# Kernel optimization log

Hardware: AMD Instinct MI355X
Metric: run time of the kernel (lower is better)

The kernel has to match this reference:

```python
import jax, jax.numpy as jnp
import numpy as np

B, T, D = 2, 2048, 2048
H, HD = 8, 128
C = H * HD  # 1024 channels
BT = 64     # chunk size
EPS_RMS = 1.1920929e-07  # torch fp32 finfo eps (RMSNorm default)


def causal_dw_conv(x, w, b):
    # x: [B,T,C], w: [C,4], b: [C]. Equals torch Conv1d(groups=C, k=4, padding=3)[..., :T]
    Bx, Tx, Cx = x.shape
    xp = jnp.pad(x, ((0, 0), (3, 0), (0, 0)))
    out = sum(xp[:, j:j + Tx, :] * w[None, None, :, j] for j in range(4))
    return out + b


def chunk_kda(q, k, v, g):
    # q,k,g: [B,H,T,K]; v: [B,H,T,V]
    Bx, Hx, Tx, K = q.shape
    V = v.shape[-1]
    NT = Tx // BT
    resh = lambda a: a.reshape(Bx, Hx, NT, BT, a.shape[-1])
    q, k, v, g = map(resh, (q, k, v, g))
    gc = jnp.cumsum(g, axis=-2)                        # [B,H,NT,BT,K]
    diff = gc[..., :, None, :] - gc[..., None, :, :]   # [B,H,NT,BT,BT,K]
    tri_incl = jnp.tril(jnp.ones((BT, BT), bool))
    tri_strict = jnp.tril(jnp.ones((BT, BT), bool), -1)
    Aqk = jnp.einsum('bhnik,bhnjk,bhnijk->bhnij', q, k, jnp.exp(diff)) * tri_incl
    Akk = jnp.einsum('bhnik,bhnjk,bhnijk->bhnij', k, k, jnp.exp(-diff)) * tri_strict
    # UT transform: the in-place forward substitution in the source computes
    # A = (I + strictly_lower(Akk))^{-1}; apply it via a unit-lower triangular solve.
    M = Akk + jnp.eye(BT, dtype=q.dtype)
    rhs = jnp.concatenate([jnp.exp(gc) * k, v], axis=-1)
    sol = jax.scipy.linalg.solve_triangular(M, rhs, lower=True, unit_diagonal=True)
    w_, u = sol[..., :K], sol[..., K:]                 # w = A@(exp(gc)*k), u = A@v
    qg = q * jnp.exp(gc)

    def step(S, xs):
        qg_i, k_i, u_i, gc_i, w_i, Aqk_i = xs
        o_i = qg_i @ S + Aqk_i @ (u_i - w_i @ S)
        g_last = gc_i[:, :, -1]                        # [B,H,K]
        decay = jnp.exp(g_last[:, :, None, :] - gc_i)  # [B,H,BT,K]
        S = S * jnp.exp(g_last)[..., :, None] + jnp.einsum('bhck,bhcv->bhkv', k_i * decay, u_i)
        return S, o_i

    xs = tuple(jnp.moveaxis(a, 2, 0) for a in (qg, k, u, gc, w_, Aqk))
    S0 = jnp.zeros((Bx, Hx, K, V), q.dtype)
    S, o = jax.lax.scan(step, S0, xs)
    o = jnp.moveaxis(o, 0, 2).reshape(Bx, Hx, Tx, V)
    return o, S


def _forward(x, Wq, Wk, Wv, conv_q_w, conv_q_b, conv_k_w, conv_k_b, conv_v_w, conv_v_b,
             Wad, Wau, Wb, Wgd, Wgu, norm_w, Wo):
    Bx, Tx, Dx = x.shape
    heads = lambda y: y.reshape(Bx, Tx, H, HD).transpose(0, 2, 1, 3)
    q = heads(causal_dw_conv(x @ Wq, conv_q_w, conv_q_b))
    k = heads(causal_dw_conv(x @ Wk, conv_k_w, conv_k_b))
    q = q / jnp.maximum(jnp.linalg.norm(q, axis=-1, keepdims=True), 1e-12)
    k = k / jnp.maximum(jnp.linalg.norm(k, axis=-1, keepdims=True), 1e-12)
    v = heads(jax.nn.silu(causal_dw_conv(x @ Wv, conv_v_w, conv_v_b)))
    alpha = jax.nn.sigmoid(heads(x @ Wad @ Wau))
    g = jnp.log(jnp.clip(alpha, 1e-6, None))
    _beta = jax.nn.sigmoid(x @ Wb)  # computed in source but unused by chunk_kda
    o, S = chunk_kda(q, k, v, g)
    o = o.transpose(0, 2, 1, 3)                        # [B,T,H,HD]
    o = o * jax.lax.rsqrt(jnp.mean(o * o, axis=-1, keepdims=True) + EPS_RMS) * norm_w
    gate = jax.nn.sigmoid(x @ Wgd @ Wgu).reshape(Bx, Tx, H, HD)
    o = (o * gate).reshape(Bx, Tx, H * HD)
    return o @ Wo, S


def setup_inputs():
    key = jax.random.key(0)
    ks = jax.random.split(key, 16)
    n = lambda k, shape, s=0.02: jax.random.normal(k, shape, jnp.float32) * s
    return {
        'x': jax.random.normal(ks[0], (B, T, D), jnp.float32),
        'Wq': n(ks[1], (D, C)), 'Wk': n(ks[2], (D, C)), 'Wv': n(ks[3], (D, C)),
        'conv_q_w': n(ks[4], (C, 4), 0.1), 'conv_q_b': jnp.zeros((C,), jnp.float32),
        'conv_k_w': n(ks[5], (C, 4), 0.1), 'conv_k_b': jnp.zeros((C,), jnp.float32),
        'conv_v_w': n(ks[6], (C, 4), 0.1), 'conv_v_b': jnp.zeros((C,), jnp.float32),
        'Wad': n(ks[7], (D, HD)), 'Wau': n(ks[8], (HD, C)),
        'Wb': n(ks[9], (D, H)),
        'Wgd': n(ks[10], (D, HD)), 'Wgu': n(ks[11], (HD, C)),
        'norm_w': jnp.ones((HD,), jnp.float32),
        'Wo': n(ks[12], (C, D)),
    }


def reference(x, Wq, Wk, Wv, conv_q_w, conv_q_b, conv_k_w, conv_k_b, conv_v_w, conv_v_b,
              Wad, Wau, Wb, Wgd, Wgu, norm_w, Wo):
    return _forward(x, Wq, Wk, Wv, conv_q_w, conv_q_b, conv_k_w, conv_k_b, conv_v_w, conv_v_b,
                    Wad, Wau, Wb, Wgd, Wgu, norm_w, Wo)
```

## Files before the change

kernel.cpp:

```cpp
#include <hip/hip_runtime.h>
#include <hip/hip_bf16.h>
#include <cstdint>
#include <cstddef>

constexpr int B_  = 2;
constexpr int T_  = 2048;
constexpr int D_  = 2048;
constexpr int H_  = 8;
constexpr int HD_ = 128;
constexpr int C_  = 1024;
constexpr int BT_ = 64;
constexpr int NT_ = 32;
constexpr int M_  = 4096;
constexpr float EPS_RMS = 1.1920929e-07f;

typedef __bf16 bf16x8 __attribute__((ext_vector_type(8)));
typedef float f32x4 __attribute__((ext_vector_type(4)));

typedef const __attribute__((address_space(1))) unsigned int* gptr_t;
typedef __attribute__((address_space(3))) unsigned int* lptr_t;

__device__ __forceinline__ void gload16(const void* g, void* l) {
  __builtin_amdgcn_global_load_lds((gptr_t)g, (lptr_t)l, 16, 0, 0);
}

template <typename OutT>
__global__ __launch_bounds__(256) void gemm_bf16k(
    const __hip_bfloat16* __restrict__ A, const __hip_bfloat16* __restrict__ Bt,
    OutT* __restrict__ C, int N, int K) {
  __shared__ __hip_bfloat16 sA[128 * 32];
  __shared__ __hip_bfloat16 sB[128 * 32];
  const int tid = threadIdx.x;
  const int lane = tid & 63;
  const int m0 = blockIdx.y * 128, n0 = blockIdx.x * 128;
  const int wm = ((tid >> 6) >> 1) * 64, wn = ((tid >> 6) & 1) * 64;
  f32x4 acc[4][4];
#pragma unroll
  for (int i = 0; i < 4; ++i)
#pragma unroll
    for (int j = 0; j < 4; ++j) acc[i][j] = (f32x4)(0.f);
  const int f0 = tid, f1 = tid + 256;
  const int r0 = f0 >> 2, c0 = (f0 & 3) * 8;
  const int r1 = f1 >> 2, c1 = (f1 & 3) * 8;
  const size_t aoff0 = (size_t)(m0 + r0) * K + c0;
  const size_t aoff1 = (size_t)(m0 + r1) * K + c1;
  const size_t boff0 = (size_t)(n0 + r0) * K + c0;
  const size_t boff1 = (size_t)(n0 + r1) * K + c1;
  const int lr = lane & 15, lk = (lane >> 4) * 8;
  for (int k0 = 0; k0 < K; k0 += 32) {
    __syncthreads();
    gload16(A + aoff0 + k0, &sA[f0 * 8]);
    gload16(A + aoff1 + k0, &sA[f1 * 8]);
    gload16(Bt + boff0 + k0, &sB[f0 * 8]);
    gload16(Bt + boff1 + k0, &sB[f1 * 8]);
    __syncthreads();
    bf16x8 af[4], bfr[4];
#pragma unroll
    for (int i = 0; i < 4; ++i)
      af[i] = *(const bf16x8*)&sA[(wm + i * 16 + lr) * 32 + lk];
#pragma unroll
    for (int j = 0; j < 4; ++j)
      bfr[j] = *(const bf16x8*)&sB[(wn + j * 16 + lr) * 32 + lk];
#pragma unroll
    for (int i = 0; i < 4; ++i)
#pragma unroll
      for (int j = 0; j < 4; ++j)
        acc[i][j] = __builtin_amdgcn_mfma_f32_16x16x32_bf16(af[i], bfr[j], acc[i][j], 0, 0, 0);
  }
  const int er = (lane >> 4) * 4, ec = lane & 15;
#pragma unroll
  for (int i = 0; i < 4; ++i) {
#pragma unroll
    for (int j = 0; j < 4; ++j) {
      int row = m0 + wm + i * 16 + er;
      int col = n0 + wn + j * 16 + ec;
#pragma unroll
      for (int r = 0; r < 4; ++r) {
        float v = acc[i][j][r];
        if constexpr (sizeof(OutT) == 2)
          C[(size_t)(row + r) * N + col] = __float2bfloat16(v);
        else
          C[(size_t)(row + r) * N + col] = v;
      }
    }
  }
}

__global__ __launch_bounds__(256) void gemm_p1(
    const __hip_bfloat16* __restrict__ xb, const __hip_bfloat16* __restrict__ Wt_qkv,
    const __hip_bfloat16* __restrict__ Wt_dg, __hip_bfloat16* __restrict__ pre_qkv,
    float* __restrict__ slabs) {
  __shared__ __hip_bfloat16 sA[128 * 32];
  __shared__ __hip_bfloat16 sB[128 * 32];
  const int bid = blockIdx.x;
  const int tid = threadIdx.x;
  const int lane = tid & 63;
  const bool isqkv = bid < 768;
  int m0, n0, kb, ke, N, z = 0;
  const __hip_bfloat16* Bt;
  if (isqkv) {
    n0 = (bid % 24) * 128; m0 = (bid / 24) * 128;
    kb = 0; ke = 2048; N = 3072; Bt = Wt_qkv;
  } else {
    int s = bid - 768;
    n0 = (s & 1) * 128; m0 = ((s >> 1) & 31) * 128;
    z = s >> 6;
    kb = z * 512; ke = kb + 512; N = 256; Bt = Wt_dg;
  }
  const int K = 2048;
  const int wm = ((tid >> 6) >> 1) * 64, wn = ((tid >> 6) & 1) * 64;
  f32x4 acc[4][4];
#pragma unroll
  for (int i = 0; i < 4; ++i)
#pragma unroll
    for (int j = 0; j < 4; ++j) acc[i][j] = (f32x4)(0.f);
  const int f0 = tid, f1 = tid + 256;
  const int r0 = f0 >> 2, c0 = (f0 & 3) * 8;
  const int r1 = f1 >> 2, c1 = (f1 & 3) * 8;
  const size_t aoff0 = (size_t)(m0 + r0) * K + c0;
  const size_t aoff1 = (size_t)(m0 + r1) * K + c1;
  const size_t boff0 = (size_t)(n0 + r0) * K + c0;
  const size_t boff1 = (size_t)(n0 + r1) * K + c1;
  const int lr = lane & 15, lk = (lane >> 4) * 8;
  for (int k0 = kb; k0 < ke; k0 += 32) {
    __syncthreads();
    gload16(xb + aoff0 + k0, &sA[f0 * 8]);
    gload16(xb + aoff1 + k0, &sA[f1 * 8]);
    gload16(Bt + boff0 + k0, &sB[f0 * 8]);
    gload16(Bt + boff1 + k0, &sB[f1 * 8]);
    __syncthreads();
    bf16x8 af[4], bfr[4];
#pragma unroll
    for (int i = 0; i < 4; ++i)
      af[i] = *(const bf16x8*)&sA[(wm + i * 16 + lr) * 32 + lk];
#pragma unroll
    for (int j = 0; j < 4; ++j)
      bfr[j] = *(const bf16x8*)&sB[(wn + j * 16 + lr) * 32 + lk];
#pragma unroll
    for (int i = 0; i < 4; ++i)
#pragma unroll
      for (int j = 0; j < 4; ++j)
        acc[i][j] = __builtin_amdgcn_mfma_f32_16x16x32_bf16(af[i], bfr[j], acc[i][j], 0, 0, 0);
  }
  const int er = (lane >> 4) * 4, ec = lane & 15;
  if (isqkv) {
#pragma unroll
    for (int i = 0; i < 4; ++i)
#pragma unroll
      for (int j = 0; j < 4; ++j) {
        int row = m0 + wm + i * 16 + er;
        int col = n0 + wn + j * 16 + ec;
#pragma unroll
        for (int r = 0; r < 4; ++r)
          pre_qkv[(size_t)(row + r) * N + col] = __float2bfloat16(acc[i][j][r]);
      }
  } else {
    float* Cs = slabs + (size_t)z * M_ * 256;
#pragma unroll
    for (int i = 0; i < 4; ++i)
#pragma unroll
      for (int j = 0; j < 4; ++j) {
        int row = m0 + wm + i * 16 + er;
        int col = n0 + wn + j * 16 + ec;
#pragma unroll
        for (int r = 0; r < 4; ++r)
          Cs[(size_t)(row + r) * N + col] = acc[i][j][r];
      }
  }
}

__global__ __launch_bounds__(256) void gemm_augu(
    const __hip_bfloat16* __restrict__ ad, const __hip_bfloat16* __restrict__ gd,
    const __hip_bfloat16* __restrict__ Wau, const __hip_bfloat16* __restrict__ Wgu,
    float* __restrict__ a_full, __hip_bfloat16* __restrict__ gatef) {
  constexpr int N = 1024, K = 128;
  const int z = blockIdx.z;
  const __hip_bfloat16* A = z ? gd : ad;
  const __hip_bfloat16* Bt = z ? Wgu : Wau;
  __shared__ __hip_bfloat16 sA[128 * 32];
  __shared__ __hip_bfloat16 sB[128 * 32];
  const int tid = threadIdx.x;
  const int lane = tid & 63;
  const int m0 = blockIdx.y * 128, n0 = blockIdx.x * 128;
  const int wm = ((tid >> 6) >> 1) * 64, wn = ((tid >> 6) & 1) * 64;
  f32x4 acc[4][4];
#pragma unroll
  for (int i = 0; i < 4; ++i)
#pragma unroll
    for (int j = 0; j < 4; ++j) acc[i][j] = (f32x4)(0.f);
  const int f0 = tid, f1 = tid + 256;
  const int r0 = f0 >> 2, c0 = (f0 & 3) * 8;
  const int r1 = f1 >> 2, c1 = (f1 & 3) * 8;
  const size_t aoff0 = (size_t)(m0 + r0) * K + c0;
  const size_t aoff1 = (size_t)(m0 + r1) * K + c1;
  const size_t boff0 = (size_t)(n0 + r0) * K + c0;
  const size_t boff1 = (size_t)(n0 + r1) * K + c1;
  const int lr = lane & 15, lk = (lane >> 4) * 8;
#pragma unroll
  for (int k0 = 0; k0 < K; k0 += 32) {
    __syncthreads();
    gload16(A + aoff0 + k0, &sA[f0 * 8]);
    gload16(A + aoff1 + k0, &sA[f1 * 8]);
    gload16(Bt + boff0 + k0, &sB[f0 * 8]);
    gload16(Bt + boff1 + k0, &sB[f1 * 8]);
    __syncthreads();
    bf16x8 af[4], bfr[4];
#pragma unroll
    for (int i = 0; i < 4; ++i)
      af[i] = *(const bf16x8*)&sA[(wm + i * 16 + lr) * 32 + lk];
#pragma unroll
    for (int j = 0; j < 4; ++j)
      bfr[j] = *(const bf16x8*)&sB[(wn + j * 16 + lr) * 32 + lk];
#pragma unroll
    for (int i = 0; i < 4; ++i)
#pragma unroll
      for (int j = 0; j < 4; ++j)
        acc[i][j] = __builtin_amdgcn_mfma_f32_16x16x32_bf16(af[i], bfr[j], acc[i][j], 0, 0, 0);
  }
  const int er = (lane >> 4) * 4, ec = lane & 15;
#pragma unroll
  for (int i = 0; i < 4; ++i)
#pragma unroll
    for (int j = 0; j < 4; ++j) {
      int row = m0 + wm + i * 16 + er;
      int col = n0 + wn + j * 16 + ec;
#pragma unroll
      for (int r = 0; r < 4; ++r) {
        float v = acc[i][j][r];
        if (z == 0) a_full[(size_t)(row + r) * N + col] = v;
        else        gatef[(size_t)(row + r) * N + col] = __float2bfloat16(v);
      }
    }
}

__global__ __launch_bounds__(256) void reduce_dg(
    const float* __restrict__ slabs, __hip_bfloat16* __restrict__ adb,
    __hip_bfloat16* __restrict__ gdb) {
  int idx = blockIdx.x * 256 + threadIdx.x;
  int m = idx >> 8, c = idx & 255;
  const size_t ss = (size_t)M_ * 256;
  float s = slabs[idx] + slabs[idx + ss] + slabs[idx + 2 * ss] + slabs[idx + 3 * ss];
  if (c < 128) adb[(size_t)m * 128 + c] = __float2bfloat16(s);
  else         gdb[(size_t)m * 128 + (c - 128)] = __float2bfloat16(s);
}

__global__ __launch_bounds__(256) void prep(
    const float* __restrict__ x, const float* __restrict__ Wq,
    const float* __restrict__ Wk, const float* __restrict__ Wv,
    const float* __restrict__ Wad, const float* __restrict__ Wgd,
    const float* __restrict__ Wau, const float* __restrict__ Wgu,
    const float* __restrict__ Wo, __hip_bfloat16* __restrict__ xb,
    __hip_bfloat16* __restrict__ Wt_qkv, __hip_bfloat16* __restrict__ Wt_dg,
    __hip_bfloat16* __restrict__ Wt_aug, __hip_bfloat16* __restrict__ Wt_o) {
  __shared__ float tile[32][33];
  int bid = blockIdx.x;
  const int tid = threadIdx.x;
  if (bid < 8192) {
    size_t i = ((size_t)bid * 256 + tid) * 4;
    float4 v = *(const float4*)(x + i);
    xb[i + 0] = __float2bfloat16(v.x);
    xb[i + 1] = __float2bfloat16(v.y);
    xb[i + 2] = __float2bfloat16(v.z);
    xb[i + 3] = __float2bfloat16(v.w);
    return;
  }
  bid -= 8192;
  const float* W; __hip_bfloat16* dst; int K, N, bx, by;
  if (bid < 6144) {
    int z = bid / 2048, r = bid % 2048;
    W = (z == 0) ? Wq : (z == 1) ? Wk : Wv;
    dst = Wt_qkv + (size_t)z * C_ * D_;
    K = D_; N = C_; bx = r & 31; by = r >> 5;
  } else if (bid < 6144 + 512) {
    int b2 = bid - 6144;
    int z = b2 >> 8, r = b2 & 255;
    W = z ? Wgd : Wad;
    dst = Wt_dg + (size_t)z * HD_ * D_;
    K = D_; N = HD_; bx = r & 3; by = r >> 2;
  } else if (bid < 6144 + 512 + 256) {
    int b2 = bid - 6144 - 512;
    int z = b2 >> 7, r = b2 & 127;
    W = z ? Wgu : Wau;
    dst = Wt_aug + (size_t)z * C_ * HD_;
    K = HD_; N = C_; bx = r & 31; by = r >> 5;
  } else {
    int b2 = bid - 6144 - 512 - 256;
    W = Wo; dst = Wt_o;
    K = C_; N = D_; bx = b2 & 63; by = b2 >> 6;
  }
  int tx = tid & 31, ty = tid >> 5;
  int kb = by * 32, nb = bx * 32;
#pragma unroll
  for (int s = 0; s < 4; ++s) {
    int kk = ty + s * 8;
    tile[kk][tx] = W[(size_t)(kb + kk) * N + nb + tx];
  }
  __syncthreads();
#pragma unroll
  for (int s = 0; s < 4; ++s) {
    int nn = ty + s * 8;
    dst[(size_t)(nb + nn) * K + kb + tx] = __float2bfloat16(tile[tx][nn]);
  }
}

__global__ __launch_bounds__(256) void gc_lds(
    const float* __restrict__ a_full, float* __restrict__ gc,
    float* __restrict__ glast) {
  __shared__ float gcS[64][128];
  const int tid = threadIdx.x;
  const int bhn = blockIdx.x;
  const int bh = bhn >> 5, n = bhn & 31;
  const int b = bh >> 3, h = bh & 7;
  const int t0 = n * 64, hoff = h * 128;
  for (int ci = tid; ci < 2048; ci += 256) {
    int r = ci >> 5, c4 = (ci & 31) * 4;
    *(float4*)&gcS[r][c4] =
        *(const float4*)(a_full + (size_t)(b * T_ + t0 + r) * C_ + hoff + c4);
  }
  __syncthreads();
  if (tid < 128) {
    float run = 0.f;
    for (int i = 0; i < 64; ++i) {
      float a = gcS[i][tid];
      float s = fmaxf(1.f / (1.f + __expf(-a)), 1e-6f);
      run += __logf(s);
      gcS[i][tid] = run;
    }
    glast[(size_t)bhn * 128 + tid] = run;
  }
  __syncthreads();
  const size_t gbase = ((size_t)bh * T_ + t0) * 128;
  for (int ci = tid; ci < 2048; ci += 256) {
    int r = ci >> 5, c4 = (ci & 31) * 4;
    *(float4*)(gc + gbase + r * 128 + c4) = *(const float4*)&gcS[r][c4];
  }
}

__global__ __launch_bounds__(128) void conv_qkv(
    const __hip_bfloat16* __restrict__ pre, const float* __restrict__ gc,
    const float* __restrict__ cqw, const float* __restrict__ cqb,
    const float* __restrict__ ckw, const float* __restrict__ ckb,
    const float* __restrict__ cvw, const float* __restrict__ cvb,
    __hip_bfloat16* __restrict__ qg, __hip_bfloat16* __restrict__ kp,
    __hip_bfloat16* __restrict__ km, __hip_bfloat16* __restrict__ vb) {
  int idx = blockIdx.x;
  int h = idx & 7;
  int t = (idx >> 3) & (T_ - 1);
  int b = idx >> 14;
  int d = threadIdx.x;
  int c = h * HD_ + d;
  const __hip_bfloat16* p = pre + (size_t)(b * T_ + t) * (3 * C_) + c;
  float aq, ak, av;
  {
    float w0 = cqw[c * 4], w1 = cqw[c * 4 + 1], w2 = cqw[c * 4 + 2], w3 = cqw[c * 4 + 3];
    aq = cqb[c] + w3 * __bfloat162float(p[0]);
    if (t > 0) aq += w2 * __bfloat162float(p[-(ptrdiff_t)(3 * C_)]);
    if (t > 1) aq += w1 * __bfloat162float(p[-2 * (ptrdiff_t)(3 * C_)]);
    if (t > 2) aq += w0 * __bfloat162float(p[-3 * (ptrdiff_t)(3 * C_)]);
  }
  {
    const __hip_bfloat16* pk = p + C_;
    float w0 = ckw[c * 4], w1 = ckw[c * 4 + 1], w2 = ckw[c * 4 + 2], w3 = ckw[c * 4 + 3];
    ak = ckb[c] + w3 * __bfloat162float(pk[0]);
    if (t > 0) ak += w2 * __bfloat162float(pk[-(ptrdiff_t)(3 * C_)]);
    if (t > 1) ak += w1 * __bfloat162float(pk[-2 * (ptrdiff_t)(3 * C_)]);
    if (t > 2) ak += w0 * __bfloat162float(pk[-3 * (ptrdiff_t)(3 * C_)]);
  }
  {
    const __hip_bfloat16* pv = p + 2 * C_;
    float w0 = cvw[c * 4], w1 = cvw[c * 4 + 1], w2 = cvw[c * 4 + 2], w3 = cvw[c * 4 + 3];
    av = cvb[c] + w3 * __bfloat162float(pv[0]);
    if (t > 0) av += w2 * __bfloat162float(pv[-(ptrdiff_t)(3 * C_)]);
    if (t > 1) av += w1 * __bfloat162float(pv[-2 * (ptrdiff_t)(3 * C_)]);
    if (t > 2) av += w0 * __bfloat162float(pv[-3 * (ptrdiff_t)(3 * C_)]);
  }
  float ssq = aq * aq, ssk = ak * ak;
#pragma unroll
  for (int o = 1; o < 64; o <<= 1) {
    ssq += __shfl_xor(ssq, o);
    ssk += __shfl_xor(ssk, o);
  }
  __shared__ float red[2][2];
  if ((d & 63) == 0) { red[0][d >> 6] = ssq; red[1][d >> 6] = ssk; }
  __syncthreads();
  float nq = fmaxf(sqrtf(red[0][0] + red[0][1]), 1e-12f);
  float nk = fmaxf(sqrtf(red[1][0] + red[1][1]), 1e-12f);
  size_t oi = (((size_t)b * H_ + h) * T_ + t) * HD_ + d;
  float g = gc[oi];
  float eg = __expf(g), emg = __expf(-g);
  qg[oi] = __float2bfloat16(aq / nq * eg);
  float kn = ak / nk;
  kp[oi] = __float2bfloat16(kn * eg);
  km[oi] = __float2bfloat16(kn * emg);
  vb[oi] = __float2bfloat16(av * (1.f / (1.f + __expf(-av))));
}

__global__ __launch_bounds__(256) void chunk_mid(
    const __hip_bfloat16* __restrict__ qg, const __hip_bfloat16* __restrict__ kp,
    const __hip_bfloat16* __restrict__ km, const __hip_bfloat16* __restrict__ vb,
    __hip_bfloat16* __restrict__ Aq, __hip_bfloat16* __restrict__ w_bf,
    __hip_bfloat16* __restrict__ u_bf, __hip_bfloat16* __restrict__ PT_bf) {
  __shared__ float A_T[64][68];
  __shared__ float solu[64][128];
  const int tid = threadIdx.x;
  const int bhn = blockIdx.x;
  const size_t gbase = ((size_t)(bhn >> 5) * T_ + (size_t)(bhn & 31) * BT_) * HD_;
  const int wv = tid >> 6, lane = tid & 63;
  const int lr = lane & 15, lg = lane >> 4;
  const int prod = wv >> 1, rh = wv & 1;

  {
    const __hip_bfloat16* A = (prod ? qg : km) + gbase;
    const __hip_bfloat16* Bt = (prod ? km : kp) + gbase;
    f32x4 acc[2][4];
#pragma unroll
    for (int i = 0; i < 2; ++i)
#pragma unroll
      for (int j = 0; j < 4; ++j) acc[i][j] = (f32x4)(0.f);
#pragma unroll
    for (int k0 = 0; k0 < 128; k0 += 32) {
      bf16x8 af[2], bfr[4];
#pragma unroll
      for (int i = 0; i < 2; ++i)
        af[i] = *(const bf16x8*)(A + (size_t)(rh * 32 + i * 16 + lr) * 128 + k0 + lg * 8);
#pragma unroll
      for (int j = 0; j < 4; ++j)
        bfr[j] = *(const bf16x8*)(Bt + (size_t)(j * 16 + lr) * 128 + k0 + lg * 8);
#pragma unroll
      for (int i = 0; i < 2; ++i)
#pragma unroll
        for (int j = 0; j < 4; ++j)
          acc[i][j] = __builtin_amdgcn_mfma_f32_16x16x32_bf16(af[i], bfr[j], acc[i][j], 0, 0, 0);
    }
    if (prod == 0) {
#pragma unroll
      for (int i = 0; i < 2; ++i)
#pragma unroll
        for (int j = 0; j < 4; ++j) {
          int row0 = rh * 32 + i * 16 + lg * 4;
          int col = j * 16 + lr;
          *(float4*)&A_T[col][row0] =
              make_float4(acc[i][j][0], acc[i][j][1], acc[i][j][2], acc[i][j][3]);
        }
    } else {
      __hip_bfloat16* dst = Aq + (size_t)bhn * 4096;
#pragma unroll
      for (int i = 0; i < 2; ++i)
#pragma unroll
        for (int j = 0; j < 4; ++j)
#pragma unroll
          for (int r = 0; r < 4; ++r) {
            int row = rh * 32 + i * 16 + lg * 4 + r;
            int col = j * 16 + lr;
            float v = (col <= row) ? acc[i][j][r] : 0.f;
            dst[row * 64 + col] = __float2bfloat16(v);
          }
    }
  }
  __syncthreads();

  {
    const int col = tid & 127;
    const __hip_bfloat16* rhs = ((tid < 128) ? kp : vb) + gbase;
    float s[64];
#pragma unroll
    for (int i = 0; i < 64; ++i)
      s[i] = __bfloat162float(rhs[(size_t)i * 128 + col]);
#pragma unroll
    for (int i = 0; i < 63; ++i) {
      const float si = s[i];
      const int j0 = (i + 1) & ~3;
#pragma unroll
      for (int j4 = j0; j4 < 64; j4 += 4) {
        float4 a4 = *(const float4*)&A_T[i][j4];
        if (j4 > i)     s[j4]     -= a4.x * si;
        if (j4 + 1 > i) s[j4 + 1] -= a4.y * si;
        if (j4 + 2 > i) s[j4 + 2] -= a4.z * si;
        if (j4 + 3 > i) s[j4 + 3] -= a4.w * si;
      }
    }
    if (tid < 128) {
#pragma unroll
      for (int i = 0; i < 64; ++i)
        w_bf[gbase + (size_t)i * 128 + col] = __float2bfloat16(s[i]);
    } else {
#pragma unroll
      for (int i = 0; i < 64; ++i) {
        u_bf[gbase + (size_t)i * 128 + col] = __float2bfloat16(s[i]);
        solu[i][col] = s[i];
      }
    }
  }
  __syncthreads();

  {
    const int kd0 = (tid >> 4) * 8, vd0 = (tid & 15) * 8;
    float acc[8][8];
#pragma unroll
    for (int a = 0; a < 8; ++a)
#pragma unroll
      for (int b2 = 0; b2 < 8; ++b2) acc[a][b2] = 0.f;
    for (int i = 0; i < 64; ++i) {
      uint4 rawv = *(const uint4*)(km + gbase + (size_t)i * 128 + kd0);
      const __hip_bfloat16* hp = (const __hip_bfloat16*)&rawv;
      float kv[8];
#pragma unroll
      for (int e = 0; e < 8; ++e) kv[e] = __bfloat162float(hp[e]);
      float uv[8];
      *(float4*)(uv)     = *(const float4*)&solu[i][vd0];
      *(float4*)(uv + 4) = *(const float4*)&solu[i][vd0 + 4];
#pragma unroll
      for (int a = 0; a < 8; ++a)
#pragma unroll
        for (int b2 = 0; b2 < 8; ++b2) acc[a][b2] = fmaf(kv[a], uv[b2], acc[a][b2]);
    }
    __hip_bfloat16* dst = PT_bf + (size_t)bhn * 16384;
#pragma unroll
    for (int b2 = 0; b2 < 8; ++b2) {
      union { __hip_bfloat16 hx[8]; uint4 u4; } pk2;
#pragma unroll
      for (int a = 0; a < 8; ++a) pk2.hx[a] = __float2bfloat16(acc[a][b2]);
      *(uint4*)(dst + (size_t)(vd0 + b2) * 128 + kd0) = pk2.u4;
    }
  }
}

__global__ __launch_bounds__(128) void scan_pt(
    const __hip_bfloat16* __restrict__ PT_bf, const float* __restrict__ glast,
    __hip_bfloat16* __restrict__ STg, float* __restrict__ Sout) {
  int vd = blockIdx.x & 127;
  int bh = blockIdx.x >> 7;
  int kd = threadIdx.x;
  float s = 0.f;
  for (int n = 0; n < NT_; ++n) {
    size_t idx = (((size_t)bh * NT_ + n) * HD_ + vd) * HD_ + kd;
    float p = __bfloat162float(PT_bf[idx]);
    STg[idx] = __float2bfloat16(s);
    float gl = glast[((size_t)bh * NT_ + n) * 128 + kd];
    s = (s + p) * __expf(gl);
  }
  Sout[((size_t)bh * HD_ + kd) * HD_ + vd] = s;
}

__global__ __launch_bounds__(256) void chunk_tail(
    const __hip_bfloat16* __restrict__ qg_bf, const __hip_bfloat16* __restrict__ w_bf,
    const __hip_bfloat16* __restrict__ u_bf, const __hip_bfloat16* __restrict__ Aq_bf,
    const __hip_bfloat16* __restrict__ STg, const __hip_bfloat16* __restrict__ gatef,
    const float* __restrict__ normw, __hip_bfloat16* __restrict__ o2b) {
  constexpr int XTS = 72;
  __shared__ __hip_bfloat16 XT[128 * XTS];
  __shared__ float red[64][4];
  const int tid = threadIdx.x;
  const int bhn = blockIdx.x;
  const int bh = bhn >> 5, n = bhn & 31;
  const int b = bh >> 3, h = bh & 7;
  const int t0 = n * 64, hoff = h * 128;
  const size_t gbase = ((size_t)bh * T_ + t0) * 128;
  const __hip_bfloat16* Sg = STg + (size_t)bhn * 16384;

  const int wv = tid >> 6, lane = tid & 63;
  const int lr = lane & 15, lg = lane >> 4;
  f32x4 accX[4][2], accO[4][2];
#pragma unroll
  for (int i = 0; i < 4; ++i)
#pragma unroll
    for (int j = 0; j < 2; ++j) { accX[i][j] = (f32x4)(0.f); accO[i][j] = (f32x4)(0.f); }

  const __hip_bfloat16* wrow = w_bf + gbase;
  const __hip_bfloat16* qrow = qg_bf + gbase;
#pragma unroll
  for (int k0 = 0; k0 < 128; k0 += 32) {
    bf16x8 aW[4], aQ[4], bS[2];
#pragma unroll
    for (int i = 0; i < 4; ++i) {
      aW[i] = *(const bf16x8*)(wrow + (size_t)(i * 16 + lr) * 128 + k0 + lg * 8);
      aQ[i] = *(const bf16x8*)(qrow + (size_t)(i * 16 + lr) * 128 + k0 + lg * 8);
    }
#pragma unroll
    for (int j = 0; j < 2; ++j)
      bS[j] = *(const bf16x8*)(Sg + (size_t)(wv * 32 + j * 16 + lr) * 128 + k0 + lg * 8);
#pragma unroll
    for (int i = 0; i < 4; ++i)
#pragma unroll
      for (int j = 0; j < 2; ++j) {
        accX[i][j] = __builtin_amdgcn_mfma_f32_16x16x32_bf16(aW[i], bS[j], accX[i][j], 0, 0, 0);
        accO[i][j] = __builtin_amdgcn_mfma_f32_16x16x32_bf16(aQ[i], bS[j], accO[i][j], 0, 0, 0);
      }
  }

#pragma unroll
  for (int i = 0; i < 4; ++i)
#pragma unroll
    for (int j = 0; j < 2; ++j) {
      int row0 = i * 16 + lg * 4;
      int col = wv * 32 + j * 16 + lr;
      union { __hip_bfloat16 hx[4]; uint2 u2; } xv;
#pragma unroll
      for (int r = 0; r < 4; ++r) {
        float uu = __bfloat162float(u_bf[gbase + (size_t)(row0 + r) * 128 + col]);
        xv.hx[r] = __float2bfloat16(uu - accX[i][j][r]);
      }
      *(uint2*)&XT[col * XTS + row0] = xv.u2;
    }
  __syncthreads();

  const __hip_bfloat16* aqb = Aq_bf + (size_t)bhn * 4096;
#pragma unroll
  for (int k0 = 0; k0 < 64; k0 += 32) {
    bf16x8 aA[4], bX[2];
#pragma unroll
    for (int i = 0; i < 4; ++i)
      aA[i] = *(const bf16x8*)(aqb + (size_t)(i * 16 + lr) * 64 + k0 + lg * 8);
#pragma unroll
    for (int j = 0; j < 2; ++j)
      bX[j] = *(const bf16x8*)&XT[(wv * 32 + j * 16 + lr) * XTS + k0 + lg * 8];
#pragma unroll
    for (int i = 0; i < 4; ++i)
#pragma unroll
      for (int j = 0; j < 2; ++j)
        accO[i][j] = __builtin_amdgcn_mfma_f32_16x16x32_bf16(aA[i], bX[j], accO[i][j], 0, 0, 0);
  }

#pragma unroll
  for (int i = 0; i < 4; ++i)
#pragma unroll
    for (int r = 0; r < 4; ++r) {
      int row = i * 16 + lg * 4 + r;
      float o0 = accO[i][0][r], o1 = accO[i][1][r];
      float ss = o0 * o0 + o1 * o1;
#pragma unroll
      for (int o = 1; o < 16; o <<= 1) ss += __shfl_xor(ss, o);
      if (lr == 0) red[row][wv] = ss;
    }
  __syncthreads();
  float nw0 = normw[wv * 32 + lr];
  float nw1 = normw[wv * 32 + 16 + lr];
#pragma unroll
  for (int i = 0; i < 4; ++i)
#pragma unroll
    for (int r = 0; r < 4; ++r) {
      int row = i * 16 + lg * 4 + r;
      float tot = red[row][0] + red[row][1] + red[row][2] + red[row][3];
      float rms = rsqrtf(tot * (1.f / 128.f) + EPS_RMS);
      size_t orow = (size_t)(b * T_ + t0 + row) * C_ + hoff;
      int c0 = wv * 32 + lr, c1 = c0 + 16;
      float g0 = __bfloat162float(gatef[orow + c0]);
      float g1 = __bfloat162float(gatef[orow + c1]);
      float s0 = 1.f / (1.f + __expf(-g0));
      float s1 = 1.f / (1.f + __expf(-g1));
      o2b[orow + c0] = __float2bfloat16(accO[i][0][r] * rms * nw0 * s0);
      o2b[orow + c1] = __float2bfloat16(accO[i][1][r] * rms * nw1 * s1);
    }
}

extern "C" void kernel_launch(void* const* d_in, const int* in_sizes, int n_in,
                              void* d_out, int out_size, void* d_ws, size_t ws_size,
                              hipStream_t stream) {
  (void)in_sizes; (void)n_in; (void)out_size;
  const float* x    = (const float*)d_in[0];
  const float* Wq   = (const float*)d_in[1];
  const float* Wk   = (const float*)d_in[2];
  const float* Wv   = (const float*)d_in[3];
  const float* cqw  = (const float*)d_in[4];
  const float* cqb  = (const float*)d_in[5];
  const float* ckw  = (const float*)d_in[6];
  const float* ckb  = (const float*)d_in[7];
  const float* cvw  = (const float*)d_in[8];
  const float* cvb  = (const float*)d_in[9];
  const float* Wad  = (const float*)d_in[10];
  const float* Wau  = (const float*)d_in[11];
  const float* Wgd  = (const float*)d_in[13];
  const float* Wgu  = (const float*)d_in[14];
  const float* normw= (const float*)d_in[15];
  const float* Wo   = (const float*)d_in[16];

  float* outp = (float*)d_out;
  float* Sout = outp + (size_t)M_ * D_;

  const size_t SZ = (size_t)M_ * C_;

  float* ws = (float*)d_ws;
  __hip_bfloat16* pre_qkv = (__hip_bfloat16*)(ws);
  float* a_full = ws + 3 * SZ / 2;
  __hip_bfloat16* gatef = (__hip_bfloat16*)(ws + 5 * SZ / 2);
  float* gc_g = ws + 3 * SZ;
  __hip_bfloat16* qg_bf = (__hip_bfloat16*)(ws + 4 * SZ);
  __hip_bfloat16* kp_bf = (__hip_bfloat16*)(ws + 9 * SZ / 2);
  __hip_bfloat16* km_bf = (__hip_bfloat16*)(ws + 5 * SZ);
  __hip_bfloat16* v_bf  = (__hip_bfloat16*)(ws + 11 * SZ / 2);
  __hip_bfloat16* w_bf  = (__hip_bfloat16*)(ws + 6 * SZ);
  __hip_bfloat16* u_bf  = (__hip_bfloat16*)(ws + 13 * SZ / 2);
  __hip_bfloat16* Aq_bf = (__hip_bfloat16*)(ws + 7 * SZ);
  float* glast = ws + 29 * SZ / 4;
  __hip_bfloat16* PT_bf = (__hip_bfloat16*)(ws + 15 * SZ / 2);
  __hip_bfloat16* STg   = (__hip_bfloat16*)(ws + 17 * SZ / 2);
  __hip_bfloat16* xb    = (__hip_bfloat16*)(ws + 19 * SZ / 2);
  __hip_bfloat16* Wt_qkv = (__hip_bfloat16*)(ws + 21 * SZ / 2);
  size_t off = 21 * SZ / 2 + 3 * SZ / 4;
  __hip_bfloat16* Wt_dg  = (__hip_bfloat16*)(ws + off); off += 262144;
  __hip_bfloat16* Wt_aug = (__hip_bfloat16*)(ws + off); off += 131072;
  __hip_bfloat16* Wt_o   = (__hip_bfloat16*)(ws + off); off += 1048576;
  __hip_bfloat16* ad_bf  = (__hip_bfloat16*)(ws + off); off += 262144;
  __hip_bfloat16* gd_bf  = (__hip_bfloat16*)(ws + off); off += 262144;
  if (ws_size < off * sizeof(float)) return;

  float* slabs = ws + 15 * SZ / 2;
  __hip_bfloat16* o2b = (__hip_bfloat16*)a_full;
  __hip_bfloat16* Wt_au = Wt_aug;
  __hip_bfloat16* Wt_gu = Wt_aug + (size_t)C_ * HD_;

  prep<<<17152, 256, 0, stream>>>(x, Wq, Wk, Wv, Wad, Wgd, Wau, Wgu, Wo,
                                  xb, Wt_qkv, Wt_dg, Wt_aug, Wt_o);

  gemm_p1<<<1024, 256, 0, stream>>>(xb, Wt_qkv, Wt_dg, pre_qkv, slabs);
  reduce_dg<<<(int)((size_t)M_ * 256 / 256), 256, 0, stream>>>(slabs, ad_bf, gd_bf);
  gemm_augu<<<dim3(C_ / 128, M_ / 128, 2), 256, 0, stream>>>(
      ad_bf, gd_bf, Wt_au, Wt_gu, a_full, gatef);

  gc_lds<<<B_ * H_ * NT_, 256, 0, stream>>>(a_full, gc_g, glast);
  conv_qkv<<<B_ * T_ * H_, 128, 0, stream>>>(pre_qkv, gc_g, cqw, cqb, ckw, ckb,
                                             cvw, cvb, qg_bf, kp_bf, km_bf, v_bf);

  chunk_mid<<<B_ * H_ * NT_, 256, 0, stream>>>(qg_bf, kp_bf, km_bf, v_bf,
                                               Aq_bf, w_bf, u_bf, PT_bf);
  scan_pt<<<B_ * H_ * HD_, 128, 0, stream>>>(PT_bf, glast, STg, Sout);

  chunk_tail<<<B_ * H_ * NT_, 256, 0, stream>>>(qg_bf, w_bf, u_bf, Aq_bf, STg,
                                                gatef, normw, o2b);
  gemm_bf16k<float><<<dim3(D_ / 128, M_ / 128), 256, 0, stream>>>(o2b, Wt_o, outp, D_, C_);
}
```

Before: 401.8 us.

## Replace projection GEMM and split-K reduce with fused 256x256 pipelined kernel

The QKV projection and the low-rank down-projections (ad/gd) now run as one 4096x3328x2048 GEMM. It uses 256x256 tiles, 8 waves, 128KB of double-buffered swizzled LDS, direct global-to-LDS loads interleaved with MFMA phases, and s_setprio scheduling. This removes the split-K fp32 slab writes, the separate reduce kernel, and the small-tile 128x128 single-buffered loop. The B pointer reads 3328 rows from Wt_qkv, so it depends on Wt_dg being laid out contiguously after Wt_qkv in the workspace (which the offsets appear to satisfy). It also launches only 208 blocks at one block per CU.

```diff
diff --git a/kernel.cpp b/kernel.cpp
--- a/kernel.cpp
+++ b/kernel.cpp
@@ -22,6 +22,176 @@
 
 __device__ __forceinline__ void gload16(const void* g, void* l) {
   __builtin_amdgcn_global_load_lds((gptr_t)g, (lptr_t)l, 16, 0, 0);
+}
+
+
+#define LD_A(base, mq, dst) do { \
+    _Pragma("unroll") for (int i_ = 0; i_ < 4; ++i_) \
+      _Pragma("unroll") for (int k_ = 0; k_ < 2; ++k_) \
+        dst[i_][k_] = *(const bf16x8*)((base) + (mq) * 8192 + i_ * 2048 + k_ * 1024); \
+  } while (0)
+
+#define LD_B(base, nq, dst) do { \
+    _Pragma("unroll") for (int j_ = 0; j_ < 2; ++j_) \
+      _Pragma("unroll") for (int k_ = 0; k_ < 2; ++k_) \
+        dst[j_][k_] = *(const bf16x8*)((base) + (nq) * 4096 + j_ * 2048 + k_ * 1024); \
+  } while (0)
+
+#define MM_Q(afr, bfr, mq, nq) do { \
+    _Pragma("unroll") for (int i_ = 0; i_ < 4; ++i_) \
+      _Pragma("unroll") for (int j_ = 0; j_ < 2; ++j_) \
+        _Pragma("unroll") for (int k_ = 0; k_ < 2; ++k_) \
+          acc[(mq) * 4 + i_][(nq) * 2 + j_] = __builtin_amdgcn_mfma_f32_16x16x32_bf16( \
+              afr[i_][k_], bfr[j_][k_], acc[(mq) * 4 + i_][(nq) * 2 + j_], 0, 0, 0); \
+  } while (0)
+
+#define STAGE(src, grow0, kc, loff) do { \
+    gload16((src) + (size_t)((grow0) + sr0) * 2048 + (kc) + sc0, smem + (loff) + tid * 16); \
+    gload16((src) + (size_t)((grow0) + sr1) * 2048 + (kc) + sc1, smem + (loff) + 8192 + tid * 16); \
+  } while (0)
+
+#define PH_SYNC_PRE do { \
+    __builtin_amdgcn_s_barrier(); \
+    asm volatile("s_waitcnt lgkmcnt(0)" ::: "memory"); \
+    __builtin_amdgcn_sched_barrier(0); \
+    __builtin_amdgcn_s_setprio(1); \
+  } while (0)
+
+#define PH_SYNC_POST do { \
+    __builtin_amdgcn_s_setprio(0); \
+    __builtin_amdgcn_sched_barrier(0); \
+    __builtin_amdgcn_s_barrier(); \
+  } while (0)
+
+#define PH_SYNC_POST_VM4 do { \
+    __builtin_amdgcn_s_setprio(0); \
+    __builtin_amdgcn_sched_barrier(0); \
+    asm volatile("s_waitcnt vmcnt(4)" ::: "memory"); \
+    __builtin_amdgcn_s_barrier(); \
+  } while (0)
+
+#define PH_SYNC_POST_VM0 do { \
+    __builtin_amdgcn_s_setprio(0); \
+    __builtin_amdgcn_sched_barrier(0); \
+    asm volatile("s_waitcnt vmcnt(0)" ::: "memory"); \
+    __builtin_amdgcn_s_barrier(); \
+  } while (0)
+
+__global__ __launch_bounds__(512, 1) void gemm8p(
+    const __hip_bfloat16* __restrict__ A_, const __hip_bfloat16* __restrict__ B_,
+    __hip_bfloat16* __restrict__ pre, __hip_bfloat16* __restrict__ adb,
+    __hip_bfloat16* __restrict__ gdb) {
+  __shared__ alignas(16) char smem[131072];
+  const int tid = threadIdx.x, lane = tid & 63;
+  const int wid = tid >> 6;
+  const int wm = (wid >> 2) * 128, wn = (wid & 3) * 64;
+  const int lr = lane & 15, lg = lane >> 4;
+
+  const int bid = blockIdx.x;
+  const int swz = (bid & 7) * 26 + (bid >> 3);
+  const int mt = swz / 13, nt = swz % 13;
+  const int m0 = mt * 256, n0g = nt * 256;
+
+  int ob0 = tid * 16;         ob0 ^= ((ob0 >> 9) & 1) << 5;
+  int ob1 = (tid + 512) * 16; ob1 ^= ((ob1 >> 9) & 1) << 5;
+  const int sr0 = ((ob0 >> 11) << 4) + ((ob0 >> 6) & 15);
+  const int sc0 = ((ob0 >> 10) & 1) * 32 + ((ob0 & 63) >> 1);
+  const int sr1 = ((ob1 >> 11) << 4) + ((ob1 >> 6) & 15);
+  const int sc1 = ((ob1 >> 10) & 1) * 32 + ((ob1 & 63) >> 1);
+
+  const int foff = lr * 64 + ((lg * 16) ^ ((lr & 8) << 2));
+  const int bq = (wn & 64) * 128;
+  const char* a0base = smem + (wm >> 7) * 16384 + foff;
+  const char* a1base = smem + 65536 + (wm >> 7) * 16384 + foff;
+  const char* b0base = smem + 32768 + (wn >> 7) * 16384 + bq + foff;
+  const char* b1base = smem + 98304 + (wn >> 7) * 16384 + bq + foff;
+
+  f32x4 acc[8][4];
+#pragma unroll
+  for (int i = 0; i < 8; ++i)
+#pragma unroll
+    for (int j = 0; j < 4; ++j) acc[i][j] = (f32x4)(0.f);
+
+  bf16x8 a[4][2], b01[2][2], b23[2][2];
+
+  STAGE(A_, m0,        0, 0);
+  STAGE(A_, m0 + 128,  0, 16384);
+  STAGE(B_, n0g,       0, 32768);
+  STAGE(B_, n0g + 128, 0, 32768 + 16384);
+  STAGE(B_, n0g,       64, 98304);
+  STAGE(B_, n0g + 128, 64, 98304 + 16384);
+  asm volatile("s_waitcnt vmcnt(4)" ::: "memory");
+  __builtin_amdgcn_s_barrier();
+
+#pragma unroll 1
+  for (int it = 0; it < 15; ++it) {
+    const int kA1 = (2 * it + 1) * 64;
+    const int kN2 = (2 * it + 2) * 64;
+    const int kB3 = (2 * it + 3) * 64;
+    LD_A(a0base, 0, a);
+    LD_B(b0base, 0, b01);
+    STAGE(A_, m0, kA1, 65536);
+    PH_SYNC_PRE; MM_Q(a, b01, 0, 0); PH_SYNC_POST;
+    LD_B(b0base, 1, b23);
+    STAGE(A_, m0 + 128, kA1, 65536 + 16384);
+    PH_SYNC_PRE; MM_Q(a, b23, 0, 1); PH_SYNC_POST;
+    LD_A(a0base, 1, a);
+    STAGE(B_, n0g, kN2, 32768);
+    PH_SYNC_PRE; MM_Q(a, b23, 1, 1); PH_SYNC_POST;
+    STAGE(B_, n0g + 128, kN2, 32768 + 16384);
+    PH_SYNC_PRE; MM_Q(a, b01, 1, 0); PH_SYNC_POST_VM4;
+    LD_A(a1base, 0, a);
+    LD_B(b1base, 0, b01);
+    STAGE(A_, m0, kN2, 0);
+    PH_SYNC_PRE; MM_Q(a, b01, 0, 0); PH_SYNC_POST;
+    LD_B(b1base, 1, b23);
+    STAGE(A_, m0 + 128, kN2, 16384);
+    PH_SYNC_PRE; MM_Q(a, b23, 0, 1); PH_SYNC_POST;
+    LD_A(a1base, 1, a);
+    STAGE(B_, n0g, kB3, 98304);
+    PH_SYNC_PRE; MM_Q(a, b23, 1, 1); PH_SYNC_POST;
+    STAGE(B_, n0g + 128, kB3, 98304 + 16384);
+    PH_SYNC_PRE; MM_Q(a, b01, 1, 0); PH_SYNC_POST_VM4;
+  }
+
+  {
+    const int kT = 1984;
+    LD_A(a0base, 0, a);
+    LD_B(b0base, 0, b01);
+    STAGE(A_, m0, kT, 65536);
+    PH_SYNC_PRE; MM_Q(a, b01, 0, 0); PH_SYNC_POST;
+    LD_B(b0base, 1, b23);
+    STAGE(A_, m0 + 128, kT, 65536 + 16384);
+    PH_SYNC_PRE; MM_Q(a, b23, 0, 1); PH_SYNC_POST;
+    LD_A(a0base, 1, a);
+    PH_SYNC_PRE; MM_Q(a, b23, 1, 1); PH_SYNC_POST;
+    PH_SYNC_PRE; MM_Q(a, b01, 1, 0); PH_SYNC_POST_VM0;
+    LD_A(a1base, 0, a);
+    LD_B(b1base, 0, b01);
+    MM_Q(a, b01, 0, 0);
+    LD_B(b1base, 1, b23);
+    MM_Q(a, b23, 0, 1);
+    LD_A(a1base, 1, a);
+    MM_Q(a, b23, 1, 1);
+    MM_Q(a, b01, 1, 0);
+  }
+
+#pragma unroll
+  for (int mf = 0; mf < 8; ++mf) {
+    const int row0 = m0 + wm + mf * 16 + lg * 4;
+#pragma unroll
+    for (int nf = 0; nf < 4; ++nf) {
+      const int c = n0g + wn + nf * 16 + lr;
+#pragma unroll
+      for (int r = 0; r < 4; ++r) {
+        const __hip_bfloat16 v = __float2bfloat16(acc[mf][nf][r]);
+        const size_t rr = (size_t)(row0 + r);
+        if (c < 3072)      pre[rr * 3072 + c] = v;
+        else if (c < 3200) adb[rr * 128 + (c - 3072)] = v;
+        else               gdb[rr * 128 + (c - 3200)] = v;
+      }
+    }
+  }
 }
 
 template <typename OutT>
@@ -86,89 +256,6 @@
   }
 }
 
-__global__ __launch_bounds__(256) void gemm_p1(
-    const __hip_bfloat16* __restrict__ xb, const __hip_bfloat16* __restrict__ Wt_qkv,
-    const __hip_bfloat16* __restrict__ Wt_dg, __hip_bfloat16* __restrict__ pre_qkv,
-    float* __restrict__ slabs) {
-  __shared__ __hip_bfloat16 sA[128 * 32];
-  __shared__ __hip_bfloat16 sB[128 * 32];
-  const int bid = blockIdx.x;
-  const int tid = threadIdx.x;
-  const int lane = tid & 63;
-  const bool isqkv = bid < 768;
-  int m0, n0, kb, ke, N, z = 0;
-  const __hip_bfloat16* Bt;
-  if (isqkv) {
-    n0 = (bid % 24) * 128; m0 = (bid / 24) * 128;
-    kb = 0; ke = 2048; N = 3072; Bt = Wt_qkv;
-  } else {
-    int s = bid - 768;
-    n0 = (s & 1) * 128; m0 = ((s >> 1) & 31) * 128;
-    z = s >> 6;
-    kb = z * 512; ke = kb + 512; N = 256; Bt = Wt_dg;
-  }
-  const int K = 2048;
-  const int wm = ((tid >> 6) >> 1) * 64, wn = ((tid >> 6) & 1) * 64;
-  f32x4 acc[4][4];
-#pragma unroll
-  for (int i = 0; i < 4; ++i)
-#pragma unroll
-    for (int j = 0; j < 4; ++j) acc[i][j] = (f32x4)(0.f);
-  const int f0 = tid, f1 = tid + 256;
-  const int r0 = f0 >> 2, c0 = (f0 & 3) * 8;
-  const int r1 = f1 >> 2, c1 = (f1 & 3) * 8;
-  const size_t aoff0 = (size_t)(m0 + r0) * K + c0;
-  const size_t aoff1 = (size_t)(m0 + r1) * K + c1;
-  const size_t boff0 = (size_t)(n0 + r0) * K + c0;
-  const size_t boff1 = (size_t)(n0 + r1) * K + c1;
-  const int lr = lane & 15, lk = (lane >> 4) * 8;
-  for (int k0 = kb; k0 < ke; k0 += 32) {
-    __syncthreads();
-    gload16(xb + aoff0 + k0, &sA[f0 * 8]);
-    gload16(xb + aoff1 + k0, &sA[f1 * 8]);
-    gload16(Bt + boff0 + k0, &sB[f0 * 8]);
-    gload16(Bt + boff1 + k0, &sB[f1 * 8]);
-    __syncthreads();
-    bf16x8 af[4], bfr[4];
-#pragma unroll
-    for (int i = 0; i < 4; ++i)
-      af[i] = *(const bf16x8*)&sA[(wm + i * 16 + lr) * 32 + lk];
-#pragma unroll
-    for (int j = 0; j < 4; ++j)
-      bfr[j] = *(const bf16x8*)&sB[(wn + j * 16 + lr) * 32 + lk];
-#pragma unroll
-    for (int i = 0; i < 4; ++i)
-#pragma unroll
-      for (int j = 0; j < 4; ++j)
-        acc[i][j] = __builtin_amdgcn_mfma_f32_16x16x32_bf16(af[i], bfr[j], acc[i][j], 0, 0, 0);
-  }
-  const int er = (lane >> 4) * 4, ec = lane & 15;
-  if (isqkv) {
-#pragma unroll
-    for (int i = 0; i < 4; ++i)
-#pragma unroll
-      for (int j = 0; j < 4; ++j) {
-        int row = m0 + wm + i * 16 + er;
-        int col = n0 + wn + j * 16 + ec;
-#pragma unroll
-        for (int r = 0; r < 4; ++r)
-          pre_qkv[(size_t)(row + r) * N + col] = __float2bfloat16(acc[i][j][r]);
-      }
-  } else {
-    float* Cs = slabs + (size_t)z * M_ * 256;
-#pragma unroll
-    for (int i = 0; i < 4; ++i)
-#pragma unroll
-      for (int j = 0; j < 4; ++j) {
-        int row = m0 + wm + i * 16 + er;
-        int col = n0 + wn + j * 16 + ec;
-#pragma unroll
-        for (int r = 0; r < 4; ++r)
-          Cs[(size_t)(row + r) * N + col] = acc[i][j][r];
-      }
-  }
-}
-
 __global__ __launch_bounds__(256) void gemm_augu(
     const __hip_bfloat16* __restrict__ ad, const __hip_bfloat16* __restrict__ gd,
     const __hip_bfloat16* __restrict__ Wau, const __hip_bfloat16* __restrict__ Wgu,
@@ -231,17 +318,6 @@
         else        gatef[(size_t)(row + r) * N + col] = __float2bfloat16(v);
       }
     }
-}
-
-__global__ __launch_bounds__(256) void reduce_dg(
-    const float* __restrict__ slabs, __hip_bfloat16* __restrict__ adb,
-    __hip_bfloat16* __restrict__ gdb) {
-  int idx = blockIdx.x * 256 + threadIdx.x;
-  int m = idx >> 8, c = idx & 255;
-  const size_t ss = (size_t)M_ * 256;
-  float s = slabs[idx] + slabs[idx + ss] + slabs[idx + 2 * ss] + slabs[idx + 3 * ss];
-  if (c < 128) adb[(size_t)m * 128 + c] = __float2bfloat16(s);
-  else         gdb[(size_t)m * 128 + (c - 128)] = __float2bfloat16(s);
 }
 
 __global__ __launch_bounds__(256) void prep(
@@ -704,7 +780,6 @@
   __hip_bfloat16* gd_bf  = (__hip_bfloat16*)(ws + off); off += 262144;
   if (ws_size < off * sizeof(float)) return;
 
-  float* slabs = ws + 15 * SZ / 2;
   __hip_bfloat16* o2b = (__hip_bfloat16*)a_full;
   __hip_bfloat16* Wt_au = Wt_aug;
   __hip_bfloat16* Wt_gu = Wt_aug + (size_t)C_ * HD_;
@@ -712,8 +787,7 @@
   prep<<<17152, 256, 0, stream>>>(x, Wq, Wk, Wv, Wad, Wgd, Wau, Wgu, Wo,
                                   xb, Wt_qkv, Wt_dg, Wt_aug, Wt_o);
 
-  gemm_p1<<<1024, 256, 0, stream>>>(xb, Wt_qkv, Wt_dg, pre_qkv, slabs);
-  reduce_dg<<<(int)((size_t)M_ * 256 / 256), 256, 0, stream>>>(slabs, ad_bf, gd_bf);
+  gemm8p<<<208, 512, 0, stream>>>(xb, Wt_qkv, pre_qkv, ad_bf, gd_bf);
   gemm_augu<<<dim3(C_ / 128, M_ / 128, 2), 256, 0, stream>>>(
       ad_bf, gd_bf, Wt_au, Wt_gu, a_full, gatef);
 
```

After: 488.2 us. 21.5% more time.
